# Kernel tuning notes

Hardware: AMD Instinct MI355X
Metric: run time of the kernel (lower is better)

Reference implementation:

```python
import jax, jax.numpy as jnp
import numpy as np

HIDDEN_DIM = 4096
EXPANSION = 4
SINKHORN_ITERS = 20
EPS = 1e-05
ALPHA_INIT = 0.01


def setup_inputs() -> dict:
    key = jax.random.key(0)
    k_x, k_res = jax.random.split(key)
    x = jax.random.normal(k_x, (4096, EXPANSION, HIDDEN_DIM), dtype=jnp.float32)
    rmsnorm_weight = jnp.ones((HIDDEN_DIM,), dtype=jnp.bfloat16)
    H_pre = jnp.zeros((EXPANSION,), dtype=jnp.float32)
    H_post = jnp.zeros((EXPANSION,), dtype=jnp.float32)
    H_res = ALPHA_INIT * jax.random.normal(k_res, (EXPANSION, EXPANSION), dtype=jnp.float32)
    return {"x": x, "rmsnorm_weight": rmsnorm_weight, "H_pre": H_pre,
            "H_post": H_post, "H_res": H_res}


def reference(x, rmsnorm_weight, H_pre, H_post, H_res):
    x_f32 = x.astype(jnp.float32)  # [B, n, C]
    # Pre-mix aggregation over the n expanded streams
    H_pre_act = jax.nn.sigmoid(H_pre)
    x_agg = jnp.einsum('k,bkc->bc', H_pre_act, x_f32)  # [B, C]
    # bf16 round-trip as in the original (x_agg.bfloat16().float())
    x_agg_bf = x_agg.astype(jnp.bfloat16).astype(jnp.float32)
    rms = jnp.sqrt(jnp.mean(x_agg_bf * x_agg_bf, axis=-1, keepdims=True) + EPS)
    y_norm = x_agg_bf / rms * rmsnorm_weight.astype(jnp.float32)  # [B, C]
    # Sinkhorn normalization of the tiny n x n mixing matrix
    M0 = jnp.exp(H_res.astype(jnp.float32))
    def body(M, _):
        M = M / jnp.maximum(M.sum(axis=1, keepdims=True), EPS)
        M = M / jnp.maximum(M.sum(axis=0, keepdims=True), EPS)
        return M, None
    M, _ = jax.lax.scan(body, M0, None, length=SINKHORN_ITERS)
    H_post_act = 2.0 * jax.nn.sigmoid(H_post)
    # [B, n, C]: mixed residual streams + broadcast of normalized aggregate
    out = jnp.einsum('ij,bjc->bic', M, x_f32) + H_post_act[None, :, None] * y_norm[:, None, :]
    return out
```

## Files before the change

kernel.cpp:

```cpp
#include <hip/hip_runtime.h>
#include <hip/hip_bf16.h>

constexpr int C   = 4096;
constexpr int NE  = 4;
constexpr int B   = 4096;
constexpr int THREADS = 512;
constexpr int PER = C / THREADS;
constexpr float EPSV = 1e-5f;

__device__ inline float bf16_rne(float f) {
    unsigned int u = __float_as_uint(f);
    unsigned int r = (u + 0x7FFFu + ((u >> 16) & 1u)) & 0xFFFF0000u;
    return __uint_as_float(r);
}

__global__ __launch_bounds__(THREADS)
void mhc_fused(const float* __restrict__ x,
               const float* __restrict__ w,
               const float* __restrict__ Hpre,
               const float* __restrict__ Hpost,
               const float* __restrict__ Hres,
               float* __restrict__ out) {
    const int b   = blockIdx.x;
    const int tid = threadIdx.x;
    const size_t rowbase = (size_t)b * NE * C;
    const int c0 = tid * PER;

    float xs[NE][PER];
    #pragma unroll
    for (int k = 0; k < NE; ++k) {
        const float4* p = reinterpret_cast<const float4*>(x + rowbase + (size_t)k * C + c0);
        float4 a = p[0];
        float4 bq = p[1];
        xs[k][0] = a.x;  xs[k][1] = a.y;  xs[k][2] = a.z;  xs[k][3] = a.w;
        xs[k][4] = bq.x; xs[k][5] = bq.y; xs[k][6] = bq.z; xs[k][7] = bq.w;
    }

    __shared__ float sM[NE * NE];
    __shared__ float red[THREADS / 64];

    if (tid < 64) {
        float m = (tid < 16) ? expf(Hres[tid]) : 0.0f;
        for (int it = 0; it < 20; ++it) {
            float r = m + __shfl_xor(m, 1);
            r += __shfl_xor(r, 2);
            m /= fmaxf(r, EPSV);
            float cs = m + __shfl_xor(m, 4);
            cs += __shfl_xor(cs, 8);
            m /= fmaxf(cs, EPSV);
        }
        if (tid < 16) sM[tid] = m;
    }

    const float s0 = 1.0f / (1.0f + expf(-Hpre[0]));
    const float s1 = 1.0f / (1.0f + expf(-Hpre[1]));
    const float s2 = 1.0f / (1.0f + expf(-Hpre[2]));
    const float s3 = 1.0f / (1.0f + expf(-Hpre[3]));
    float hp[NE];
    #pragma unroll
    for (int i = 0; i < NE; ++i) hp[i] = 2.0f / (1.0f + expf(-Hpost[i]));

    float aggbf[PER];
    float ss = 0.0f;
    #pragma unroll
    for (int c = 0; c < PER; ++c) {
        float a = s0 * xs[0][c] + s1 * xs[1][c] + s2 * xs[2][c] + s3 * xs[3][c];
        float abf = bf16_rne(a);
        aggbf[c] = abf;
        ss += abf * abf;
    }

    #pragma unroll
    for (int off = 32; off > 0; off >>= 1) ss += __shfl_xor(ss, off);
    const int lane = tid & 63;
    const int wid  = tid >> 6;
    if (lane == 0) red[wid] = ss;
    __syncthreads();
    float tot = 0.0f;
    #pragma unroll
    for (int i = 0; i < THREADS / 64; ++i) tot += red[i];

    const float rinv = 1.0f / sqrtf(tot * (1.0f / (float)C) + EPSV);

    float y[PER];
    {
        const float4* pw = reinterpret_cast<const float4*>(w + c0);
        float4 w0 = pw[0];
        float4 w1 = pw[1];
        y[0] = aggbf[0] * rinv * w0.x;  y[1] = aggbf[1] * rinv * w0.y;
        y[2] = aggbf[2] * rinv * w0.z;  y[3] = aggbf[3] * rinv * w0.w;
        y[4] = aggbf[4] * rinv * w1.x;  y[5] = aggbf[5] * rinv * w1.y;
        y[6] = aggbf[6] * rinv * w1.z;  y[7] = aggbf[7] * rinv * w1.w;
    }

    float M[NE][NE];
    #pragma unroll
    for (int i = 0; i < NE; ++i)
        #pragma unroll
        for (int j = 0; j < NE; ++j)
            M[i][j] = sM[i * NE + j];

    #pragma unroll
    for (int i = 0; i < NE; ++i) {
        float o[PER];
        #pragma unroll
        for (int c = 0; c < PER; ++c) {
            o[c] = M[i][0] * xs[0][c] + M[i][1] * xs[1][c]
                 + M[i][2] * xs[2][c] + M[i][3] * xs[3][c]
                 + hp[i] * y[c];
        }
        float4* po = reinterpret_cast<float4*>(out + rowbase + (size_t)i * C + c0);
        po[0] = make_float4(o[0], o[1], o[2], o[3]);
        po[1] = make_float4(o[4], o[5], o[6], o[7]);
    }
}

extern "C" void kernel_launch(void* const* d_in, const int* in_sizes, int n_in,
                              void* d_out, int out_size, void* d_ws, size_t ws_size,
                              hipStream_t stream) {
    const float* x     = (const float*)d_in[0];
    const float* w     = (const float*)d_in[1];
    const float* Hpre  = (const float*)d_in[2];
    const float* Hpost = (const float*)d_in[3];
    const float* Hres  = (const float*)d_in[4];
    float* out         = (float*)d_out;

    mhc_fused<<<B, THREADS, 0, stream>>>(x, w, Hpre, Hpost, Hres, out);
}
```

Measured before the change: 113.2 us.

## Process one row per wavefront with two-pass streaming and no block sync

Each 64-lane wavefront now owns a whole batch row and loops over it in chunks. It first computes the sum of squares, then re-reads x to produce the outputs. This drops the LDS reduction, the __syncthreads and the shared Sinkhorn matrix, since every wave runs its own Sinkhorn and broadcasts it with shuffles. The cost is reading x twice and relying on cache to keep the second read off DRAM, plus redundant Sinkhorn work in every wave.

```diff
diff --git a/kernel.cpp b/kernel.cpp
--- a/kernel.cpp
+++ b/kernel.cpp
@@ -1,11 +1,10 @@
 #include <hip/hip_runtime.h>
-#include <hip/hip_bf16.h>
 
 constexpr int C   = 4096;
 constexpr int NE  = 4;
 constexpr int B   = 4096;
-constexpr int THREADS = 512;
-constexpr int PER = C / THREADS;
+constexpr int THREADS = 256;
+constexpr int NCHUNK = C / (64 * 8);
 constexpr float EPSV = 1e-5f;
 
 __device__ inline float bf16_rne(float f) {
@@ -14,43 +13,30 @@
     return __uint_as_float(r);
 }
 
-__global__ __launch_bounds__(THREADS)
-void mhc_fused(const float* __restrict__ x,
-               const float* __restrict__ w,
-               const float* __restrict__ Hpre,
-               const float* __restrict__ Hpost,
-               const float* __restrict__ Hres,
-               float* __restrict__ out) {
-    const int b   = blockIdx.x;
-    const int tid = threadIdx.x;
-    const size_t rowbase = (size_t)b * NE * C;
-    const int c0 = tid * PER;
+__global__ __launch_bounds__(THREADS, 4)
+void mhc_wave(const float* __restrict__ x,
+              const float* __restrict__ w,
+              const float* __restrict__ Hpre,
+              const float* __restrict__ Hpost,
+              const float* __restrict__ Hres,
+              float* __restrict__ out) {
+    const int lane = threadIdx.x & 63;
+    const int row  = blockIdx.x * (THREADS / 64) + (threadIdx.x >> 6);
+    const float* xrow = x   + (size_t)row * (NE * C);
+    float*       orow = out + (size_t)row * (NE * C);
 
-    float xs[NE][PER];
+    float m = (lane < 16) ? expf(Hres[lane]) : 0.0f;
+    for (int it = 0; it < 20; ++it) {
+        float r = m + __shfl_xor(m, 1);
+        r += __shfl_xor(r, 2);
+        m /= fmaxf(r, EPSV);
+        float cs = m + __shfl_xor(m, 4);
+        cs += __shfl_xor(cs, 8);
+        m /= fmaxf(cs, EPSV);
+    }
+    float M[NE * NE];
     #pragma unroll
-    for (int k = 0; k < NE; ++k) {
-        const float4* p = reinterpret_cast<const float4*>(x + rowbase + (size_t)k * C + c0);
-        float4 a = p[0];
-        float4 bq = p[1];
-        xs[k][0] = a.x;  xs[k][1] = a.y;  xs[k][2] = a.z;  xs[k][3] = a.w;
-        xs[k][4] = bq.x; xs[k][5] = bq.y; xs[k][6] = bq.z; xs[k][7] = bq.w;
-    }
-
-    __shared__ float sM[NE * NE];
-    __shared__ float red[THREADS / 64];
-
-    if (tid < 64) {
-        float m = (tid < 16) ? expf(Hres[tid]) : 0.0f;
-        for (int it = 0; it < 20; ++it) {
-            float r = m + __shfl_xor(m, 1);
-            r += __shfl_xor(r, 2);
-            m /= fmaxf(r, EPSV);
-            float cs = m + __shfl_xor(m, 4);
-            cs += __shfl_xor(cs, 8);
-            m /= fmaxf(cs, EPSV);
-        }
-        if (tid < 16) sM[tid] = m;
-    }
+    for (int k = 0; k < NE * NE; ++k) M[k] = __shfl(m, k);
 
     const float s0 = 1.0f / (1.0f + expf(-Hpre[0]));
     const float s1 = 1.0f / (1.0f + expf(-Hpre[1]));
@@ -60,58 +46,65 @@
     #pragma unroll
     for (int i = 0; i < NE; ++i) hp[i] = 2.0f / (1.0f + expf(-Hpost[i]));
 
-    float aggbf[PER];
     float ss = 0.0f;
     #pragma unroll
-    for (int c = 0; c < PER; ++c) {
-        float a = s0 * xs[0][c] + s1 * xs[1][c] + s2 * xs[2][c] + s3 * xs[3][c];
-        float abf = bf16_rne(a);
-        aggbf[c] = abf;
-        ss += abf * abf;
+    for (int c = 0; c < NCHUNK; ++c) {
+        const int off = c * 512 + lane * 8;
+        float xv[NE][8];
+        #pragma unroll
+        for (int k = 0; k < NE; ++k) {
+            const float4* p = reinterpret_cast<const float4*>(xrow + k * C + off);
+            float4 a = p[0], bq = p[1];
+            xv[k][0] = a.x;  xv[k][1] = a.y;  xv[k][2] = a.z;  xv[k][3] = a.w;
+            xv[k][4] = bq.x; xv[k][5] = bq.y; xv[k][6] = bq.z; xv[k][7] = bq.w;
+        }
+        #pragma unroll
+        for (int e = 0; e < 8; ++e) {
+            float a = s0 * xv[0][e] + s1 * xv[1][e] + s2 * xv[2][e] + s3 * xv[3][e];
+            float abf = bf16_rne(a);
+            ss += abf * abf;
+        }
     }
 
     #pragma unroll
     for (int off = 32; off > 0; off >>= 1) ss += __shfl_xor(ss, off);
-    const int lane = tid & 63;
-    const int wid  = tid >> 6;
-    if (lane == 0) red[wid] = ss;
-    __syncthreads();
-    float tot = 0.0f;
-    #pragma unroll
-    for (int i = 0; i < THREADS / 64; ++i) tot += red[i];
 
-    const float rinv = 1.0f / sqrtf(tot * (1.0f / (float)C) + EPSV);
-
-    float y[PER];
-    {
-        const float4* pw = reinterpret_cast<const float4*>(w + c0);
-        float4 w0 = pw[0];
-        float4 w1 = pw[1];
-        y[0] = aggbf[0] * rinv * w0.x;  y[1] = aggbf[1] * rinv * w0.y;
-        y[2] = aggbf[2] * rinv * w0.z;  y[3] = aggbf[3] * rinv * w0.w;
-        y[4] = aggbf[4] * rinv * w1.x;  y[5] = aggbf[5] * rinv * w1.y;
-        y[6] = aggbf[6] * rinv * w1.z;  y[7] = aggbf[7] * rinv * w1.w;
-    }
-
-    float M[NE][NE];
-    #pragma unroll
-    for (int i = 0; i < NE; ++i)
-        #pragma unroll
-        for (int j = 0; j < NE; ++j)
-            M[i][j] = sM[i * NE + j];
+    const float rinv = 1.0f / sqrtf(ss * (1.0f / (float)C) + EPSV);
 
     #pragma unroll
-    for (int i = 0; i < NE; ++i) {
-        float o[PER];
+    for (int c = 0; c < NCHUNK; ++c) {
+        const int off = c * 512 + lane * 8;
+        float xv[NE][8];
         #pragma unroll
-        for (int c = 0; c < PER; ++c) {
-            o[c] = M[i][0] * xs[0][c] + M[i][1] * xs[1][c]
-                 + M[i][2] * xs[2][c] + M[i][3] * xs[3][c]
-                 + hp[i] * y[c];
+        for (int k = 0; k < NE; ++k) {
+            const float4* p = reinterpret_cast<const float4*>(xrow + k * C + off);
+            float4 a = p[0], bq = p[1];
+            xv[k][0] = a.x;  xv[k][1] = a.y;  xv[k][2] = a.z;  xv[k][3] = a.w;
+            xv[k][4] = bq.x; xv[k][5] = bq.y; xv[k][6] = bq.z; xv[k][7] = bq.w;
         }
-        float4* po = reinterpret_cast<float4*>(out + rowbase + (size_t)i * C + c0);
-        po[0] = make_float4(o[0], o[1], o[2], o[3]);
-        po[1] = make_float4(o[4], o[5], o[6], o[7]);
+        const float4* pw = reinterpret_cast<const float4*>(w + off);
+        float4 w0 = pw[0], w1 = pw[1];
+        float wf[8] = { w0.x, w0.y, w0.z, w0.w, w1.x, w1.y, w1.z, w1.w };
+
+        float y[8];
+        #pragma unroll
+        for (int e = 0; e < 8; ++e) {
+            float a = s0 * xv[0][e] + s1 * xv[1][e] + s2 * xv[2][e] + s3 * xv[3][e];
+            y[e] = bf16_rne(a) * rinv * wf[e];
+        }
+        #pragma unroll
+        for (int i = 0; i < NE; ++i) {
+            float o[8];
+            #pragma unroll
+            for (int e = 0; e < 8; ++e) {
+                o[e] = M[i * NE + 0] * xv[0][e] + M[i * NE + 1] * xv[1][e]
+                     + M[i * NE + 2] * xv[2][e] + M[i * NE + 3] * xv[3][e]
+                     + hp[i] * y[e];
+            }
+            float4* po = reinterpret_cast<float4*>(orow + i * C + off);
+            po[0] = make_float4(o[0], o[1], o[2], o[3]);
+            po[1] = make_float4(o[4], o[5], o[6], o[7]);
+        }
     }
 }
 
@@ -125,5 +118,5 @@
     const float* Hres  = (const float*)d_in[4];
     float* out         = (float*)d_out;
 
-    mhc_fused<<<B, THREADS, 0, stream>>>(x, w, Hpre, Hpost, Hres, out);
+    mhc_wave<<<B / (THREADS / 64), THREADS, 0, stream>>>(x, w, Hpre, Hpost, Hres, out);
 }
```

After: 239.0 us. 111% more time.

## Process four rows per block with register double-buffered prefetch

Applied to the files above, without the earlier changes.

Each block now handles four batch rows and prefetches the next row's inputs into a second register buffer while the current row's reduction and output run. This amortises the per-block Sinkhorn and weight loads and tries to overlap global loads with compute and sync. It doubles the register footprint for input tiles, which may lower occupancy, and cuts the grid to a quarter of the blocks.

```diff
diff --git a/kernel.cpp b/kernel.cpp
--- a/kernel.cpp
+++ b/kernel.cpp
@@ -1,11 +1,11 @@
 #include <hip/hip_runtime.h>
-#include <hip/hip_bf16.h>
 
 constexpr int C   = 4096;
 constexpr int NE  = 4;
 constexpr int B   = 4096;
 constexpr int THREADS = 512;
 constexpr int PER = C / THREADS;
+constexpr int RPB = 4;
 constexpr float EPSV = 1e-5f;
 
 __device__ inline float bf16_rne(float f) {
@@ -14,30 +14,32 @@
     return __uint_as_float(r);
 }
 
-__global__ __launch_bounds__(THREADS)
-void mhc_fused(const float* __restrict__ x,
-               const float* __restrict__ w,
-               const float* __restrict__ Hpre,
-               const float* __restrict__ Hpost,
-               const float* __restrict__ Hres,
-               float* __restrict__ out) {
-    const int b   = blockIdx.x;
-    const int tid = threadIdx.x;
-    const size_t rowbase = (size_t)b * NE * C;
-    const int c0 = tid * PER;
-
-    float xs[NE][PER];
+__device__ __forceinline__ void load_row(const float* __restrict__ xrow, int c0,
+                                         float (&xs)[NE][PER]) {
     #pragma unroll
     for (int k = 0; k < NE; ++k) {
-        const float4* p = reinterpret_cast<const float4*>(x + rowbase + (size_t)k * C + c0);
-        float4 a = p[0];
-        float4 bq = p[1];
+        const float4* p = reinterpret_cast<const float4*>(xrow + k * C + c0);
+        float4 a = p[0], bq = p[1];
         xs[k][0] = a.x;  xs[k][1] = a.y;  xs[k][2] = a.z;  xs[k][3] = a.w;
         xs[k][4] = bq.x; xs[k][5] = bq.y; xs[k][6] = bq.z; xs[k][7] = bq.w;
     }
+}
+
+__global__ __launch_bounds__(THREADS)
+void mhc_pipe(const float* __restrict__ x,
+              const float* __restrict__ w,
+              const float* __restrict__ Hpre,
+              const float* __restrict__ Hpost,
+              const float* __restrict__ Hres,
+              float* __restrict__ out) {
+    const int tid  = threadIdx.x;
+    const int lane = tid & 63;
+    const int wid  = tid >> 6;
+    const int c0   = tid * PER;
+    const size_t blockbase = (size_t)blockIdx.x * RPB * NE * C;
 
     __shared__ float sM[NE * NE];
-    __shared__ float red[THREADS / 64];
+    __shared__ float red[RPB][THREADS / 64];
 
     if (tid < 64) {
         float m = (tid < 16) ? expf(Hres[tid]) : 0.0f;
@@ -60,59 +62,71 @@
     #pragma unroll
     for (int i = 0; i < NE; ++i) hp[i] = 2.0f / (1.0f + expf(-Hpost[i]));
 
-    float aggbf[PER];
-    float ss = 0.0f;
-    #pragma unroll
-    for (int c = 0; c < PER; ++c) {
-        float a = s0 * xs[0][c] + s1 * xs[1][c] + s2 * xs[2][c] + s3 * xs[3][c];
-        float abf = bf16_rne(a);
-        aggbf[c] = abf;
-        ss += abf * abf;
+    float wf[PER];
+    {
+        const float4* pw = reinterpret_cast<const float4*>(w + c0);
+        float4 w0 = pw[0], w1 = pw[1];
+        wf[0] = w0.x; wf[1] = w0.y; wf[2] = w0.z; wf[3] = w0.w;
+        wf[4] = w1.x; wf[5] = w1.y; wf[6] = w1.z; wf[7] = w1.w;
     }
 
-    #pragma unroll
-    for (int off = 32; off > 0; off >>= 1) ss += __shfl_xor(ss, off);
-    const int lane = tid & 63;
-    const int wid  = tid >> 6;
-    if (lane == 0) red[wid] = ss;
-    __syncthreads();
-    float tot = 0.0f;
-    #pragma unroll
-    for (int i = 0; i < THREADS / 64; ++i) tot += red[i];
+    float xsA[NE][PER], xsB[NE][PER];
+    float M[NE * NE];
 
-    const float rinv = 1.0f / sqrtf(tot * (1.0f / (float)C) + EPSV);
-
-    float y[PER];
-    {
-        const float4* pw = reinterpret_cast<const float4*>(w + c0);
-        float4 w0 = pw[0];
-        float4 w1 = pw[1];
-        y[0] = aggbf[0] * rinv * w0.x;  y[1] = aggbf[1] * rinv * w0.y;
-        y[2] = aggbf[2] * rinv * w0.z;  y[3] = aggbf[3] * rinv * w0.w;
-        y[4] = aggbf[4] * rinv * w1.x;  y[5] = aggbf[5] * rinv * w1.y;
-        y[6] = aggbf[6] * rinv * w1.z;  y[7] = aggbf[7] * rinv * w1.w;
-    }
-
-    float M[NE][NE];
-    #pragma unroll
-    for (int i = 0; i < NE; ++i)
-        #pragma unroll
-        for (int j = 0; j < NE; ++j)
-            M[i][j] = sM[i * NE + j];
-
-    #pragma unroll
-    for (int i = 0; i < NE; ++i) {
-        float o[PER];
+    auto step = [&](int r, float (&cur)[NE][PER], float (&nxt)[NE][PER]) {
+        float ss = 0.0f;
         #pragma unroll
         for (int c = 0; c < PER; ++c) {
-            o[c] = M[i][0] * xs[0][c] + M[i][1] * xs[1][c]
-                 + M[i][2] * xs[2][c] + M[i][3] * xs[3][c]
-                 + hp[i] * y[c];
+            float a = s0 * cur[0][c] + s1 * cur[1][c] + s2 * cur[2][c] + s3 * cur[3][c];
+            float abf = bf16_rne(a);
+            ss += abf * abf;
         }
-        float4* po = reinterpret_cast<float4*>(out + rowbase + (size_t)i * C + c0);
-        po[0] = make_float4(o[0], o[1], o[2], o[3]);
-        po[1] = make_float4(o[4], o[5], o[6], o[7]);
-    }
+
+        if (r + 1 < RPB)
+            load_row(x + blockbase + (size_t)(r + 1) * NE * C, c0, nxt);
+
+        #pragma unroll
+        for (int off = 32; off > 0; off >>= 1) ss += __shfl_xor(ss, off);
+        if (lane == 0) red[r][wid] = ss;
+        __syncthreads();
+
+        if (r == 0) {
+            #pragma unroll
+            for (int k = 0; k < NE * NE; ++k) M[k] = sM[k];
+        }
+
+        float tot = 0.0f;
+        #pragma unroll
+        for (int i = 0; i < THREADS / 64; ++i) tot += red[r][i];
+        const float rinv = 1.0f / sqrtf(tot * (1.0f / (float)C) + EPSV);
+
+        float* orow = out + blockbase + (size_t)r * NE * C;
+        float y[PER];
+        #pragma unroll
+        for (int c = 0; c < PER; ++c) {
+            float a = s0 * cur[0][c] + s1 * cur[1][c] + s2 * cur[2][c] + s3 * cur[3][c];
+            y[c] = bf16_rne(a) * rinv * wf[c];
+        }
+        #pragma unroll
+        for (int i = 0; i < NE; ++i) {
+            float o[PER];
+            #pragma unroll
+            for (int c = 0; c < PER; ++c) {
+                o[c] = M[i * NE + 0] * cur[0][c] + M[i * NE + 1] * cur[1][c]
+                     + M[i * NE + 2] * cur[2][c] + M[i * NE + 3] * cur[3][c]
+                     + hp[i] * y[c];
+            }
+            float4* po = reinterpret_cast<float4*>(orow + (size_t)i * C + c0);
+            po[0] = make_float4(o[0], o[1], o[2], o[3]);
+            po[1] = make_float4(o[4], o[5], o[6], o[7]);
+        }
+    };
+
+    load_row(x + blockbase, c0, xsA);
+    step(0, xsA, xsB);
+    step(1, xsB, xsA);
+    step(2, xsA, xsB);
+    step(3, xsB, xsA);
 }
 
 extern "C" void kernel_launch(void* const* d_in, const int* in_sizes, int n_in,
@@ -125,5 +139,5 @@
     const float* Hres  = (const float*)d_in[4];
     float* out         = (float*)d_out;
 
-    mhc_fused<<<B, THREADS, 0, stream>>>(x, w, Hpre, Hpost, Hres, out);
+    mhc_pipe<<<B / RPB, THREADS, 0, stream>>>(x, w, Hpre, Hpost, Hres, out);
 }
```

After: 110.8 us. -2.1%, faster.
